# Optimization experiments

Hardware: AMD Instinct MI355X
Metric: run time of the kernel (lower is better)

Reference implementation:

```python
import jax, jax.numpy as jnp
import numpy as np

B, G, K, N, M, E, L = 8, 512, 64, 1024, 128, 4, 5

def _lin(x, w, b):
    return x @ w.T + b

def setup_inputs():
    key = jax.random.key(0)
    ks = jax.random.split(key, 20)
    def nrm(k, shape, s=1.0):
        return jax.random.normal(k, shape, dtype=jnp.float32) * s
    def lin_p(k, out_d, in_d):
        k1, k2 = jax.random.split(k)
        s = 1.0 / float(np.sqrt(in_d))
        return nrm(k1, (out_d, in_d), s), nrm(k2, (out_d,), s)
    inp = {}
    inp["z"] = nrm(ks[0], (B, G, K, M), 0.5)
    inp["hs_grid"] = nrm(ks[1], (B, G, M))
    inp["hs_key"] = nrm(ks[2], (B, K, M))
    inp["lig_rep"] = nrm(ks[3], (B, E))
    inp["hs_rec"] = nrm(ks[4], (B, N, M))
    inp["w_Rl"] = jnp.ones((1,), dtype=jnp.float32)
    inp["w_mask"] = jax.random.randint(ks[5], (B, K), 0, 2)
    dims = {"wra": (M, M), "wrh": (M, M), "wla": (M, M), "wlh": (M, M),
            "z1": (1, M), "wcR": (M, M), "wcl": (M, M), "kR": (M, M),
            "mapL": (L, 2 * M + E), "fin": (1, L)}
    for i, nm in enumerate(dims):
        w, b = lin_p(ks[6 + i], *dims[nm])
        inp[nm + "_w"] = w
        inp[nm + "_b"] = b
    return inp

def reference(z, hs_grid, hs_key, lig_rep, hs_rec, w_Rl, w_mask,
              wra_w, wra_b, wrh_w, wrh_b, wla_w, wla_b, wlh_w, wlh_b,
              z1_w, z1_b, wcR_w, wcR_b, wcl_w, wcl_b, kR_w, kR_b,
              mapL_w, mapL_b, fin_w, fin_b):
    exp_z = jnp.exp(z)                                    # [B,G,K,M]
    zr = exp_z / exp_z.sum(axis=-2, keepdims=True)        # pseudo-softmax over K
    ra = jnp.einsum('bgkm,bkm->bgm', zr, hs_key)          # [B,G,M]
    zl = exp_z / exp_z.sum(axis=-3, keepdims=True)        # pseudo-softmax over G
    la = jnp.einsum('bgkm,bgm->bkm', zl, hs_grid)         # [B,K,M]
    ra_rh = _lin(ra, wra_w, wra_b) + _lin(hs_grid, wrh_w, wrh_b)  # [B,G,M]
    la_lh = _lin(la, wla_w, wla_b) + _lin(hs_key, wlh_w, wlh_b)   # [B,K,M]
    att = _lin(z, z1_w, z1_b)[..., 0]                     # [B,G,K]
    att_l = jax.nn.softmax(att, axis=2).sum(axis=1)       # [B,K]
    att_r = jax.nn.softmax(att, axis=1).sum(axis=2)       # [B,G]
    key_rep = jnp.einsum('bk,bkm->bm', att_l, la_lh)      # [B,M]
    grid_rep = jnp.einsum('bg,bgm->bm', att_r, ra_rh)     # [B,M]
    Rh = _lin(hs_rec, wcR_w, wcR_b)                       # [B,N,M]
    lh = _lin(hs_key, wcl_w, wcl_b)                       # [B,K,M]
    z_Rl = jnp.einsum('bnh,bkh->bnk', Rh, lh)             # [B,N,K]
    masked = jnp.where(w_mask[:, None, :] == 0, jnp.float32(-1e10), w_Rl * z_Rl)
    z_Rl = jax.nn.softmax(masked, axis=1)                 # softmax over N
    kfr = jnp.einsum('bnk,bnh->bkh', z_Rl, hs_rec)        # [B,K,M]
    kfr = _lin(kfr, kR_w, kR_b)
    kfr = jnp.einsum('bk,bkh->bh', att_l, kfr)            # [B,M]
    key_rep = key_rep + kfr
    pair_rep = jnp.concatenate([key_rep, lig_rep, grid_rep], axis=1)  # [B,2M+E]
    pair_rep = _lin(pair_rep, mapL_w, mapL_b)             # [B,L]
    return _lin(pair_rep, fin_w, fin_b)[..., 0]           # [B]
```

## Files before the change

kernel.cpp:

```cpp
#include <hip/hip_runtime.h>

#define Bb 8
#define Gg 512
#define Kk 64
#define Nn 1024
#define Mm 128
#define KM (Kk * Mm)
#define GPB 16
#define NCH (Gg / GPB)

struct P7 { const float* p[7]; };

__global__ __launch_bounds__(1024) void kA(
    const float* __restrict__ z, const float* __restrict__ hs_grid,
    const float* __restrict__ hs_key, const float* __restrict__ z1w,
    P7 ptrs, float* __restrict__ wT,
    float* __restrict__ raOut, float* __restrict__ attOut,
    float* __restrict__ laNum, float* __restrict__ laDen)
{
  __shared__ __align__(16) float smem[18432];
  const int bid = blockIdx.x;
  const int t = threadIdx.x;

  if (bid >= Bb * NCH) {
    float* tile = smem;
    const int r = bid - Bb * NCH;
    const int mat = r >> 4, tl = r & 15;
    const int xo = (tl & 3) * 32, y0 = (tl >> 2) * 32;
    const int tx = t & 31, ty = t >> 5;
    const float* src = ptrs.p[mat];
    float* dst = wT + (size_t)mat * Mm * Mm;
    tile[ty * 33 + tx] = src[(size_t)(y0 + ty) * Mm + xo + tx];
    __syncthreads();
    dst[(size_t)(xo + ty) * Mm + y0 + tx] = tile[tx * 33 + ty];
    return;
  }

  float* s_hskey  = smem;
  float* s_hsgrid = smem + 8192;
  float* s_rn     = smem + 10240;
  float* s_rd     = smem + 14336;

  const int b = bid >> 5;
  const int gblk = bid & 31;
  const int lane_m = t & 31;
  const int m4 = lane_m << 2;
  const int kgrp = t >> 5;
  const int wv = t >> 6;

  const float* hkb = hs_key + (size_t)b * KM;
  for (int idx = t; idx < KM; idx += 1024) s_hskey[idx] = hkb[idx];
  const float* hgb = hs_grid + ((size_t)b * Gg + gblk * GPB) * Mm;
  for (int idx = t; idx < GPB * Mm; idx += 1024) s_hsgrid[idx] = hgb[idx];

  const float zw0 = z1w[m4], zw1 = z1w[m4 + 1], zw2 = z1w[m4 + 2], zw3 = z1w[m4 + 3];

  float la_n[2][4], la_d[2][4];
#pragma unroll
  for (int i = 0; i < 2; ++i)
#pragma unroll
    for (int j = 0; j < 4; ++j) { la_n[i][j] = 0.f; la_d[i][j] = 0.f; }

  const float* zb = z + ((size_t)b * Gg + gblk * GPB) * (size_t)Mm * Kk;
  const int ofs0 = (kgrp * 2) * Mm + m4;
  const int ofs1 = ofs0 + Mm;
  float4 c0 = *reinterpret_cast<const float4*>(zb + ofs0);
  float4 c1 = *reinterpret_cast<const float4*>(zb + ofs1);

  __syncthreads();

  for (int gl = 0; gl < GPB; ++gl) {
    float4 n0 = c0, n1 = c1;
    if (gl < GPB - 1) {
      n0 = *reinterpret_cast<const float4*>(zb + (size_t)(gl + 1) * KM + ofs0);
      n1 = *reinterpret_cast<const float4*>(zb + (size_t)(gl + 1) * KM + ofs1);
    }
    const int g = gblk * GPB + gl;
    const float4 hg = *reinterpret_cast<const float4*>(s_hsgrid + gl * Mm + m4);
    float rn0 = 0, rn1 = 0, rn2 = 0, rn3 = 0, rd0 = 0, rd1 = 0, rd2 = 0, rd3 = 0;
#pragma unroll
    for (int i = 0; i < 2; ++i) {
      const float4 v = (i == 0) ? c0 : c1;
      const int k = kgrp * 2 + i;
      const float e0 = __expf(v.x), e1 = __expf(v.y), e2 = __expf(v.z), e3 = __expf(v.w);
      la_n[i][0] += e0 * hg.x; la_n[i][1] += e1 * hg.y; la_n[i][2] += e2 * hg.z; la_n[i][3] += e3 * hg.w;
      la_d[i][0] += e0;        la_d[i][1] += e1;        la_d[i][2] += e2;        la_d[i][3] += e3;
      const float4 hk = *reinterpret_cast<const float4*>(s_hskey + k * Mm + m4);
      rn0 += e0 * hk.x; rn1 += e1 * hk.y; rn2 += e2 * hk.z; rn3 += e3 * hk.w;
      rd0 += e0; rd1 += e1; rd2 += e2; rd3 += e3;
      float ap = v.x * zw0 + v.y * zw1 + v.z * zw2 + v.w * zw3;
      ap += __shfl_xor(ap, 16); ap += __shfl_xor(ap, 8); ap += __shfl_xor(ap, 4);
      ap += __shfl_xor(ap, 2);  ap += __shfl_xor(ap, 1);
      if (lane_m == 0) attOut[((size_t)b * Gg + g) * Kk + k] = ap;
    }
    rn0 += __shfl_xor(rn0, 32); rn1 += __shfl_xor(rn1, 32); rn2 += __shfl_xor(rn2, 32); rn3 += __shfl_xor(rn3, 32);
    rd0 += __shfl_xor(rd0, 32); rd1 += __shfl_xor(rd1, 32); rd2 += __shfl_xor(rd2, 32); rd3 += __shfl_xor(rd3, 32);
    float* rnB = s_rn + (gl & 1) * 2048;
    float* rdB = s_rd + (gl & 1) * 2048;
    if ((t & 63) < 32) {
      *reinterpret_cast<float4*>(rnB + wv * Mm + m4) = make_float4(rn0, rn1, rn2, rn3);
      *reinterpret_cast<float4*>(rdB + wv * Mm + m4) = make_float4(rd0, rd1, rd2, rd3);
    }
    __syncthreads();
    if (t < Mm) {
      float num = 0.f, den = 0.f;
#pragma unroll
      for (int ww = 0; ww < 16; ++ww) { num += rnB[ww * Mm + t]; den += rdB[ww * Mm + t]; }
      raOut[((size_t)b * Gg + g) * Mm + t] = num / den;
    }
    c0 = n0; c1 = n1;
  }

  const size_t base = ((size_t)(b * NCH + gblk)) * KM;
#pragma unroll
  for (int i = 0; i < 2; ++i) {
    const int k = kgrp * 2 + i;
    *reinterpret_cast<float4*>(laNum + base + k * Mm + m4) =
        make_float4(la_n[i][0], la_n[i][1], la_n[i][2], la_n[i][3]);
    *reinterpret_cast<float4*>(laDen + base + k * Mm + m4) =
        make_float4(la_d[i][0], la_d[i][1], la_d[i][2], la_d[i][3]);
  }
}

__device__ __forceinline__ void lin1_body(
    int r0, const float* __restrict__ in1, const float* __restrict__ W1T,
    const float* __restrict__ b1, float* __restrict__ out, float* smem)
{
  float* s1 = smem;
  float* sacc = smem + 2048;
  const int t = threadIdx.x;
  const int m = t & 127, hh = t >> 7;
  for (int idx = t; idx < 2048; idx += 256) s1[idx] = in1[(size_t)r0 * Mm + idx];
  __syncthreads();
  float acc[16];
#pragma unroll
  for (int r = 0; r < 16; ++r) acc[r] = 0.f;
  const int h0 = hh * 64;
  for (int h = h0; h < h0 + 64; ++h) {
    const float w1 = W1T[(size_t)h * Mm + m];
#pragma unroll
    for (int r = 0; r < 16; ++r) acc[r] += s1[r * Mm + h] * w1;
  }
  if (hh == 1) {
#pragma unroll
    for (int r = 0; r < 16; ++r) sacc[r * Mm + m] = acc[r];
  }
  __syncthreads();
  if (hh == 0) {
    const float bias = b1[m];
#pragma unroll
    for (int r = 0; r < 16; ++r) out[(size_t)(r0 + r) * Mm + m] = acc[r] + sacc[r * Mm + m] + bias;
  }
}

__global__ __launch_bounds__(256) void kB(
    const float* __restrict__ laNum, const float* __restrict__ laDen, float* __restrict__ la,
    const float* __restrict__ att, float* __restrict__ attlP,
    float* __restrict__ attrPM, float* __restrict__ attrPS,
    const float* __restrict__ hs_rec, const float* __restrict__ hs_key,
    const float* __restrict__ wT, const float* __restrict__ wcR_b, const float* __restrict__ wcl_b,
    float* __restrict__ Rh, float* __restrict__ lh)
{
  __shared__ __align__(16) float smem[4096];
  const int bid = blockIdx.x;
  const int t = threadIdx.x;

  if (bid < 256) {
    const int idx = bid * 256 + t;
    const int b = idx >> 13, r = idx & 8191;
    const float* np = laNum + (size_t)b * NCH * KM + r;
    const float* dp = laDen + (size_t)b * NCH * KM + r;
    float num = 0.f, den = 0.f;
#pragma unroll 8
    for (int p = 0; p < NCH; ++p) { num += np[(size_t)p * KM]; den += dp[(size_t)p * KM]; }
    la[idx] = num / den;
  } else if (bid < 320) {
    const int blk = bid - 256;
    const int b = blk >> 3, p = blk & 7;
    const int w = t >> 6, lane = t & 63;
    float acc = 0.f;
    for (int j = 0; j < 16; ++j) {
      const int g = p * 64 + w * 16 + j;
      const float a = att[((size_t)b * Gg + g) * Kk + lane];
      float mx = a;
      for (int off = 32; off; off >>= 1) mx = fmaxf(mx, __shfl_xor(mx, off));
      const float e = __expf(a - mx);
      float s = e;
      for (int off = 32; off; off >>= 1) s += __shfl_xor(s, off);
      acc += e / s;
    }
    float* sred = smem;
    sred[w * 64 + lane] = acc;
    __syncthreads();
    if (t < 64) attlP[(b * 8 + p) * 64 + t] = sred[t] + sred[64 + t] + sred[128 + t] + sred[192 + t];
  } else if (bid < 384) {
    const int blk = bid - 320;
    const int b = blk >> 3, gc = blk & 7;
    const int k = t & 63, j4 = t >> 6;
    float m = -1e30f, s = 0.f;
    for (int j = 0; j < 16; ++j) {
      const int g = gc * 64 + j4 * 16 + j;
      const float a = att[((size_t)b * Gg + g) * Kk + k];
      if (a > m) { s = s * __expf(m - a) + 1.0f; m = a; }
      else s += __expf(a - m);
    }
    float* sm = smem;
    float* ss = smem + 256;
    sm[j4 * 64 + k] = m; ss[j4 * 64 + k] = s;
    __syncthreads();
    if (t < 64) {
      float M = sm[t];
      for (int q = 1; q < 4; ++q) M = fmaxf(M, sm[q * 64 + t]);
      float S = 0.f;
      for (int q = 0; q < 4; ++q) S += ss[q * 64 + t] * __expf(sm[q * 64 + t] - M);
      attrPM[(b * 8 + gc) * 64 + t] = M;
      attrPS[(b * 8 + gc) * 64 + t] = S;
    }
  } else if (bid < 896) {
    lin1_body((bid - 384) * 16, hs_rec, wT + 4 * 16384, wcR_b, Rh, smem);
  } else {
    lin1_body((bid - 896) * 16, hs_key, wT + 5 * 16384, wcl_b, lh, smem);
  }
}

__global__ __launch_bounds__(256) void kC(
    const float* __restrict__ att, const float* __restrict__ attrPM, const float* __restrict__ attrPS,
    float* __restrict__ att_r,
    const float* __restrict__ Rh, const float* __restrict__ lh,
    const int* __restrict__ mask, const float* __restrict__ wRl,
    float* __restrict__ scores, float* __restrict__ pmT, float* __restrict__ psT)
{
  __shared__ __align__(16) float smem[14912];
  const int bid = blockIdx.x;
  const int t = threadIdx.x;

  if (bid < 64) {
    const int b = bid >> 3, gc = bid & 7;
    const int k = t & 63, grp = t >> 6;
    float* Mx = smem;
    float* S = smem + 64;
    if (t < 64) {
      float M = -1e30f;
      for (int p = 0; p < 8; ++p) M = fmaxf(M, attrPM[(b * 8 + p) * 64 + t]);
      float s = 0.f;
      for (int p = 0; p < 8; ++p) s += attrPS[(b * 8 + p) * 64 + t] * __expf(attrPM[(b * 8 + p) * 64 + t] - M);
      Mx[t] = M; S[t] = s;
    }
    __syncthreads();
    const float Mk = Mx[k], Sk = S[k];
    for (int j = 0; j < 16; ++j) {
      const int g = gc * 64 + grp * 16 + j;
      float p = __expf(att[((size_t)b * Gg + g) * Kk + k] - Mk) / Sk;
      for (int off = 32; off; off >>= 1) p += __shfl_xor(p, off);
      if (k == 0) att_r[b * Gg + g] = p;
    }
  } else {
    const int vb = bid - 64;
    const int b = vb >> 6, ntile = vb & 63;
    const int n0 = ntile * 16;
    const int k = t & 63, hs = t >> 6;
    float* s_rh  = smem;
    float* s_lh  = smem + 2048;
    float* s_acc = smem + 10304;
    float* s_m   = smem + 14400;
    float* s_s   = smem + 14656;
    for (int idx = t; idx < 2048; idx += 256)
      s_rh[idx] = Rh[((size_t)b * Nn + n0) * Mm + idx];
    for (int idx = t; idx < 8192; idx += 256)
      s_lh[(idx >> 7) * 129 + (idx & 127)] = lh[(size_t)b * Kk * Mm + idx];
    __syncthreads();
    float acc[16];
#pragma unroll
    for (int r = 0; r < 16; ++r) acc[r] = 0.f;
    for (int h = hs * 32; h < hs * 32 + 32; ++h) {
      const float lv = s_lh[k * 129 + h];
#pragma unroll
      for (int r = 0; r < 16; ++r) acc[r] += s_rh[r * Mm + h] * lv;
    }
#pragma unroll
    for (int r = 0; r < 16; ++r) s_acc[(hs * 16 + r) * 64 + k] = acc[r];
    __syncthreads();
    const float wv = wRl[0];
    const bool msk = (mask[b * Kk + k] == 0);
    float m = -3.0e38f, ssum = 0.f;
    for (int q = 0; q < 4; ++q) {
      const int idx = q * 256 + t;
      const int r = idx >> 6, kk = idx & 63;
      float v = s_acc[r * 64 + kk] + s_acc[(16 + r) * 64 + kk] +
                s_acc[(32 + r) * 64 + kk] + s_acc[(48 + r) * 64 + kk];
      v = msk ? -1e10f : wv * v;
      scores[((size_t)b * Nn + n0 + r) * Kk + kk] = v;
      if (v > m) { ssum = ssum * __expf(m - v) + 1.0f; m = v; }
      else ssum += __expf(v - m);
    }
    s_m[hs * 64 + k] = m; s_s[hs * 64 + k] = ssum;
    __syncthreads();
    if (t < 64) {
      float M = fmaxf(fmaxf(s_m[t], s_m[64 + t]), fmaxf(s_m[128 + t], s_m[192 + t]));
      float S = 0.f;
#pragma unroll
      for (int q = 0; q < 4; ++q) S += s_s[q * 64 + t] * __expf(s_m[q * 64 + t] - M);
      pmT[((size_t)b * 64 + ntile) * 64 + t] = M;
      psT[((size_t)b * 64 + ntile) * 64 + t] = S;
    }
  }
}

__global__ __launch_bounds__(512) void kD(
    const float* __restrict__ scores, const float* __restrict__ hs_rec,
    const float* __restrict__ pmT, const float* __restrict__ psT,
    const float* __restrict__ attlP, const float* __restrict__ att_r,
    const float* __restrict__ ra, const float* __restrict__ hs_grid,
    const float* __restrict__ la, const float* __restrict__ hs_key,
    float* __restrict__ uP, float* __restrict__ w1P, float* __restrict__ w2P,
    float* __restrict__ w0P, float* __restrict__ v1, float* __restrict__ v2,
    float* __restrict__ sAv)
{
  __shared__ float sm[1280];
  __shared__ float s_attl[64];
  __shared__ float sM[64], sSi[64];
  const int bid = blockIdx.x;
  const int t = threadIdx.x;

  if (bid < 64) {
    const int b = bid >> 3, nc = bid & 7;
    if (t < 64) {
      float a = 0.f;
      for (int p = 0; p < 8; ++p) a += attlP[(b * 8 + p) * 64 + t];
      s_attl[t] = a;
      float M = -3.0e38f;
      for (int nt = 0; nt < 64; ++nt) M = fmaxf(M, pmT[((size_t)b * 64 + nt) * 64 + t]);
      float S = 0.f;
      for (int nt = 0; nt < 64; ++nt)
        S += psT[((size_t)b * 64 + nt) * 64 + t] * __expf(pmT[((size_t)b * 64 + nt) * 64 + t] - M);
      sM[t] = M; sSi[t] = 1.0f / S;
    }
    __syncthreads();
    const int n = t >> 2, ks = t & 3;
    const float* sc = scores + ((size_t)b * Nn + nc * 128 + n) * Kk + ks * 16;
    float qp = 0.f;
#pragma unroll
    for (int j = 0; j < 16; ++j) {
      const int k = ks * 16 + j;
      qp += s_attl[k] * __expf(sc[j] - sM[k]) * sSi[k];
    }
    sm[n * 4 + ks] = qp;
    __syncthreads();
    float* q = sm + 512;
    if (t < 128) q[t] = sm[t * 4] + sm[t * 4 + 1] + sm[t * 4 + 2] + sm[t * 4 + 3];
    __syncthreads();
    const int h = t & 127, nq = t >> 7;
    float acc = 0.f;
    const float* hr = hs_rec + ((size_t)b * Nn + nc * 128 + nq * 32) * Mm + h;
    for (int j = 0; j < 32; ++j) acc += q[nq * 32 + j] * hr[(size_t)j * Mm];
    float* red = sm + 640;
    red[nq * 128 + h] = acc;
    __syncthreads();
    if (t < 128) uP[((size_t)b * 8 + nc) * 128 + t] = red[t] + red[128 + t] + red[256 + t] + red[384 + t];
  } else if (bid < 128) {
    const int blk = bid - 64;
    const int b = blk >> 3, gc = blk & 7;
    float* s_ar = sm + 1152;
    if (t < 64) s_ar[t] = att_r[b * Gg + gc * 64 + t];
    __syncthreads();
    const int h = t & 127, gq = t >> 7;
    float a1 = 0.f, a2 = 0.f;
    const float* rp = ra + ((size_t)b * Gg + gc * 64 + gq * 16) * Mm + h;
    const float* gp = hs_grid + ((size_t)b * Gg + gc * 64 + gq * 16) * Mm + h;
    for (int j = 0; j < 16; ++j) {
      const float w = s_ar[gq * 16 + j];
      a1 += w * rp[(size_t)j * Mm];
      a2 += w * gp[(size_t)j * Mm];
    }
    float* r1 = sm;
    float* r2 = sm + 512;
    r1[gq * 128 + h] = a1; r2[gq * 128 + h] = a2;
    __syncthreads();
    if (t < 128) {
      w1P[((size_t)b * 8 + gc) * 128 + t] = r1[t] + r1[128 + t] + r1[256 + t] + r1[384 + t];
      w2P[((size_t)b * 8 + gc) * 128 + t] = r2[t] + r2[128 + t] + r2[256 + t] + r2[384 + t];
    }
    if (t == 0) {
      float s = 0.f;
      for (int j = 0; j < 64; ++j) s += s_ar[j];
      w0P[b * 8 + gc] = s;
    }
  } else {
    const int b = bid - 128;
    if (t < 64) {
      float a = 0.f;
      for (int p = 0; p < 8; ++p) a += attlP[(b * 8 + p) * 64 + t];
      s_attl[t] = a;
    }
    __syncthreads();
    const int h = t & 127, kq = t >> 7;
    float a1 = 0.f, a2 = 0.f;
    const float* lp = la + ((size_t)b * Kk + kq * 16) * Mm + h;
    const float* kp = hs_key + ((size_t)b * Kk + kq * 16) * Mm + h;
    for (int j = 0; j < 16; ++j) {
      const float w = s_attl[kq * 16 + j];
      a1 += w * lp[(size_t)j * Mm];
      a2 += w * kp[(size_t)j * Mm];
    }
    float* r1 = sm;
    float* r2 = sm + 512;
    r1[kq * 128 + h] = a1; r2[kq * 128 + h] = a2;
    __syncthreads();
    if (t < 128) {
      v1[b * 128 + t] = r1[t] + r1[128 + t] + r1[256 + t] + r1[384 + t];
      v2[b * 128 + t] = r2[t] + r2[128 + t] + r2[256 + t] + r2[384 + t];
    }
    if (t == 0) {
      float s = 0.f;
      for (int j = 0; j < 64; ++j) s += s_attl[j];
      sAv[b] = s;
    }
  }
}

__global__ __launch_bounds__(256) void kE(
    const float* __restrict__ uP, const float* __restrict__ w1P, const float* __restrict__ w2P,
    const float* __restrict__ w0P, const float* __restrict__ v1, const float* __restrict__ v2,
    const float* __restrict__ sAv, const float* __restrict__ wT,
    const float* __restrict__ wra_b, const float* __restrict__ wrh_b,
    const float* __restrict__ wla_b, const float* __restrict__ wlh_b,
    const float* __restrict__ kR_b, const float* __restrict__ lig_rep,
    const float* __restrict__ mapL_w, const float* __restrict__ mapL_b,
    const float* __restrict__ fin_w, const float* __restrict__ fin_b,
    float* __restrict__ out)
{
  __shared__ float sV1[128], sV2[128], sU[128], sW1[128], sW2[128];
  __shared__ float sPair[260];
  __shared__ float sRed[2][2][128];
  __shared__ float s5[8];
  __shared__ float sSc[2];
  const int b = blockIdx.x, t = threadIdx.x;
  const int m = t & 127, hf = t >> 7;

  if (t < 128) {
    float u = 0.f, w1 = 0.f, w2 = 0.f;
    for (int c = 0; c < 8; ++c) {
      u  += uP[((size_t)b * 8 + c) * 128 + t];
      w1 += w1P[((size_t)b * 8 + c) * 128 + t];
      w2 += w2P[((size_t)b * 8 + c) * 128 + t];
    }
    sU[t] = u; sW1[t] = w1; sW2[t] = w2;
    sV1[t] = v1[b * 128 + t]; sV2[t] = v2[b * 128 + t];
  }
  if (t == 0) {
    float s = 0.f;
    for (int c = 0; c < 8; ++c) s += w0P[b * 8 + c];
    sSc[0] = s;
    sSc[1] = sAv[b];
  }
  __syncthreads();

  const float* wraT = wT;
  const float* wrhT = wT + 1 * 16384;
  const float* wlaT = wT + 2 * 16384;
  const float* wlhT = wT + 3 * 16384;
  const float* kRT  = wT + 6 * 16384;
  float key = 0.f, grd = 0.f;
  for (int h = hf * 64; h < hf * 64 + 64; ++h) {
    key += sV1[h] * wlaT[h * Mm + m] + sV2[h] * wlhT[h * Mm + m] + sU[h] * kRT[h * Mm + m];
    grd += sW1[h] * wraT[h * Mm + m] + sW2[h] * wrhT[h * Mm + m];
  }
  sRed[0][hf][m] = key; sRed[1][hf][m] = grd;
  __syncthreads();
  if (t < 128) {
    const float sR = sSc[0], sA = sSc[1];
    sPair[t] = sRed[0][0][t] + sRed[0][1][t] + sA * (wla_b[t] + wlh_b[t] + kR_b[t]);
    sPair[132 + t] = sRed[1][0][t] + sRed[1][1][t] + sR * (wra_b[t] + wrh_b[t]);
  }
  if (t < 4) sPair[128 + t] = lig_rep[b * 4 + t];
  __syncthreads();

  const int wv = t >> 6, lane = t & 63;
  for (int l = wv; l < 5; l += 4) {
    float acc = 0.f;
    for (int c = lane; c < 260; c += 64) acc += sPair[c] * mapL_w[l * 260 + c];
    for (int off = 32; off; off >>= 1) acc += __shfl_xor(acc, off);
    if (lane == 0) s5[l] = acc + mapL_b[l];
  }
  __syncthreads();
  if (t == 0) {
    float o = fin_b[0];
    for (int l = 0; l < 5; ++l) o += s5[l] * fin_w[l];
    out[b] = o;
  }
}

extern "C" void kernel_launch(void* const* d_in, const int* in_sizes, int n_in,
                              void* d_out, int out_size, void* d_ws, size_t ws_size,
                              hipStream_t stream) {
  const float* z       = (const float*)d_in[0];
  const float* hs_grid = (const float*)d_in[1];
  const float* hs_key  = (const float*)d_in[2];
  const float* lig_rep = (const float*)d_in[3];
  const float* hs_rec  = (const float*)d_in[4];
  const float* w_Rl    = (const float*)d_in[5];
  const int*   w_mask  = (const int*)d_in[6];
  const float* wra_w = (const float*)d_in[7];  const float* wra_b = (const float*)d_in[8];
  const float* wrh_w = (const float*)d_in[9];  const float* wrh_b = (const float*)d_in[10];
  const float* wla_w = (const float*)d_in[11]; const float* wla_b = (const float*)d_in[12];
  const float* wlh_w = (const float*)d_in[13]; const float* wlh_b = (const float*)d_in[14];
  const float* z1_w  = (const float*)d_in[15];
  const float* wcR_w = (const float*)d_in[17]; const float* wcR_b = (const float*)d_in[18];
  const float* wcl_w = (const float*)d_in[19]; const float* wcl_b = (const float*)d_in[20];
  const float* kR_w  = (const float*)d_in[21]; const float* kR_b  = (const float*)d_in[22];
  const float* mapL_w = (const float*)d_in[23]; const float* mapL_b = (const float*)d_in[24];
  const float* fin_w  = (const float*)d_in[25]; const float* fin_b  = (const float*)d_in[26];
  float* out = (float*)d_out;

  float* w = (float*)d_ws;
  float* wT    = w;
  float* ra    = wT + 7 * 16384;
  float* att   = ra + Bb * Gg * Mm;
  float* laNum = att + Bb * Gg * Kk;
  float* laDen = laNum + Bb * NCH * Kk * Mm;
  float* la    = laDen + Bb * NCH * Kk * Mm;
  float* attlP = la + Bb * Kk * Mm;
  float* attrPM = attlP + Bb * 8 * 64;
  float* attrPS = attrPM + Bb * 8 * 64;
  float* att_r = attrPS + Bb * 8 * 64;
  float* Rh    = att_r + Bb * Gg;
  float* lh    = Rh + Bb * Nn * Mm;
  float* scores = lh + Bb * Kk * Mm;

  float* pmT  = laNum;
  float* psT  = laNum + 32768;
  float* uP   = laNum + 65536;
  float* w1P  = laNum + 73728;
  float* w2P  = laNum + 81920;
  float* w0P  = laNum + 90112;
  float* v1   = laNum + 90176;
  float* v2   = laNum + 91200;
  float* sAv  = laNum + 92224;

  P7 ptrs;
  ptrs.p[0] = wra_w; ptrs.p[1] = wrh_w; ptrs.p[2] = wla_w; ptrs.p[3] = wlh_w;
  ptrs.p[4] = wcR_w; ptrs.p[5] = wcl_w; ptrs.p[6] = kR_w;

  kA<<<Bb * NCH + 112, 1024, 0, stream>>>(z, hs_grid, hs_key, z1_w, ptrs, wT,
                                          ra, att, laNum, laDen);
  kB<<<928, 256, 0, stream>>>(laNum, laDen, la, att, attlP, attrPM, attrPS,
                              hs_rec, hs_key, wT, wcR_b, wcl_b, Rh, lh);
  kC<<<576, 256, 0, stream>>>(att, attrPM, attrPS, att_r, Rh, lh,
                              w_mask, w_Rl, scores, pmT, psT);
  kD<<<136, 512, 0, stream>>>(scores, hs_rec, pmT, psT, attlP, att_r,
                              ra, hs_grid, la, hs_key,
                              uP, w1P, w2P, w0P, v1, v2, sAv);
  kE<<<Bb, 256, 0, stream>>>(uP, w1P, w2P, w0P, v1, v2, sAv, wT,
                             wra_b, wrh_b, wla_b, wlh_b, kR_b, lig_rep,
                             mapL_w, mapL_b, fin_w, fin_b, out);
}
```

Measured before the change: 89.20 us.

## Reassociate receptor-key scores to skip projecting hs_rec through wcR

The scores are rewritten as hs_rec · (lh·wcR_w), so a small per-key matrix Lk of shape [B,K,M] is computed instead of the full [B,N,M] projection Rh. The wcR bias term is dropped. It only adds a per-(b,k) constant that cancels in the softmax over N, as long as the stored scores and their max/sum stay consistent. kB loses 480 blocks of GEMM work. kC now reads hs_rec directly from global memory with per-thread register copies of Lk, instead of staging both operands in shared memory. The trade-offs are less data reuse from LDS in kC and scores that differ numerically by that constant offset.

```diff
diff --git a/kernel.cpp b/kernel.cpp
--- a/kernel.cpp
+++ b/kernel.cpp
@@ -122,46 +122,15 @@
   }
 }
 
-__device__ __forceinline__ void lin1_body(
-    int r0, const float* __restrict__ in1, const float* __restrict__ W1T,
-    const float* __restrict__ b1, float* __restrict__ out, float* smem)
-{
-  float* s1 = smem;
-  float* sacc = smem + 2048;
-  const int t = threadIdx.x;
-  const int m = t & 127, hh = t >> 7;
-  for (int idx = t; idx < 2048; idx += 256) s1[idx] = in1[(size_t)r0 * Mm + idx];
-  __syncthreads();
-  float acc[16];
-#pragma unroll
-  for (int r = 0; r < 16; ++r) acc[r] = 0.f;
-  const int h0 = hh * 64;
-  for (int h = h0; h < h0 + 64; ++h) {
-    const float w1 = W1T[(size_t)h * Mm + m];
-#pragma unroll
-    for (int r = 0; r < 16; ++r) acc[r] += s1[r * Mm + h] * w1;
-  }
-  if (hh == 1) {
-#pragma unroll
-    for (int r = 0; r < 16; ++r) sacc[r * Mm + m] = acc[r];
-  }
-  __syncthreads();
-  if (hh == 0) {
-    const float bias = b1[m];
-#pragma unroll
-    for (int r = 0; r < 16; ++r) out[(size_t)(r0 + r) * Mm + m] = acc[r] + sacc[r * Mm + m] + bias;
-  }
-}
-
 __global__ __launch_bounds__(256) void kB(
     const float* __restrict__ laNum, const float* __restrict__ laDen, float* __restrict__ la,
     const float* __restrict__ att, float* __restrict__ attlP,
     float* __restrict__ attrPM, float* __restrict__ attrPS,
-    const float* __restrict__ hs_rec, const float* __restrict__ hs_key,
-    const float* __restrict__ wT, const float* __restrict__ wcR_b, const float* __restrict__ wcl_b,
-    float* __restrict__ Rh, float* __restrict__ lh)
+    const float* __restrict__ hs_key, const float* __restrict__ wT,
+    const float* __restrict__ wcR_w, const float* __restrict__ wcl_b,
+    float* __restrict__ Lk)
 {
-  __shared__ __align__(16) float smem[4096];
+  __shared__ __align__(16) float smem[1088];
   const int bid = blockIdx.x;
   const int t = threadIdx.x;
 
@@ -216,21 +185,63 @@
       attrPM[(b * 8 + gc) * 64 + t] = M;
       attrPS[(b * 8 + gc) * 64 + t] = S;
     }
-  } else if (bid < 896) {
-    lin1_body((bid - 384) * 16, hs_rec, wT + 4 * 16384, wcR_b, Rh, smem);
   } else {
-    lin1_body((bid - 896) * 16, hs_key, wT + 5 * 16384, wcl_b, lh, smem);
+    const int blk = bid - 384;
+    const int b = blk >> 3, k8 = blk & 7;
+    float* s_lh = smem;
+    const int m = t & 127;
+    const int half = __builtin_amdgcn_readfirstlane(t >> 7);
+    const float* wclT = wT + 5 * 16384;
+    {
+      const float* keyb = hs_key + ((size_t)b * Kk + k8 * 8 + half * 4) * Mm;
+      float a0 = 0.f, a1 = 0.f, a2 = 0.f, a3 = 0.f;
+      for (int h = 0; h < 128; ++h) {
+        const float w = wclT[(size_t)h * Mm + m];
+        const float r0v = keyb[h];
+        const float r1v = keyb[128 + h];
+        const float r2v = keyb[256 + h];
+        const float r3v = keyb[384 + h];
+        a0 += r0v * w; a1 += r1v * w; a2 += r2v * w; a3 += r3v * w;
+      }
+      const float bm = wcl_b[m];
+      s_lh[(half * 4 + 0) * 132 + m] = a0 + bm;
+      s_lh[(half * 4 + 1) * 132 + m] = a1 + bm;
+      s_lh[(half * 4 + 2) * 132 + m] = a2 + bm;
+      s_lh[(half * 4 + 3) * 132 + m] = a3 + bm;
+    }
+    __syncthreads();
+    {
+      const int h = m;
+      const int r0 = half * 4;
+      float b0 = 0.f, b1 = 0.f, b2 = 0.f, b3 = 0.f;
+      for (int mq = 0; mq < 32; ++mq) {
+        const float4 L0 = *reinterpret_cast<const float4*>(&s_lh[(r0 + 0) * 132 + mq * 4]);
+        const float4 L1 = *reinterpret_cast<const float4*>(&s_lh[(r0 + 1) * 132 + mq * 4]);
+        const float4 L2 = *reinterpret_cast<const float4*>(&s_lh[(r0 + 2) * 132 + mq * 4]);
+        const float4 L3 = *reinterpret_cast<const float4*>(&s_lh[(r0 + 3) * 132 + mq * 4]);
+        const float w0 = wcR_w[(size_t)(mq * 4 + 0) * Mm + h];
+        const float w1 = wcR_w[(size_t)(mq * 4 + 1) * Mm + h];
+        const float w2 = wcR_w[(size_t)(mq * 4 + 2) * Mm + h];
+        const float w3 = wcR_w[(size_t)(mq * 4 + 3) * Mm + h];
+        b0 += L0.x * w0 + L0.y * w1 + L0.z * w2 + L0.w * w3;
+        b1 += L1.x * w0 + L1.y * w1 + L1.z * w2 + L1.w * w3;
+        b2 += L2.x * w0 + L2.y * w1 + L2.z * w2 + L2.w * w3;
+        b3 += L3.x * w0 + L3.y * w1 + L3.z * w2 + L3.w * w3;
+      }
+      const size_t ob = ((size_t)b * Kk + k8 * 8 + r0) * Mm + h;
+      Lk[ob] = b0; Lk[ob + Mm] = b1; Lk[ob + 2 * Mm] = b2; Lk[ob + 3 * Mm] = b3;
+    }
   }
 }
 
 __global__ __launch_bounds__(256) void kC(
     const float* __restrict__ att, const float* __restrict__ attrPM, const float* __restrict__ attrPS,
     float* __restrict__ att_r,
-    const float* __restrict__ Rh, const float* __restrict__ lh,
+    const float* __restrict__ hs_rec, const float* __restrict__ Lk,
     const int* __restrict__ mask, const float* __restrict__ wRl,
     float* __restrict__ scores, float* __restrict__ pmT, float* __restrict__ psT)
 {
-  __shared__ __align__(16) float smem[14912];
+  __shared__ __align__(16) float smem[4608];
   const int bid = blockIdx.x;
   const int t = threadIdx.x;
 
@@ -258,27 +269,33 @@
     const int vb = bid - 64;
     const int b = vb >> 6, ntile = vb & 63;
     const int n0 = ntile * 16;
-    const int k = t & 63, hs = t >> 6;
-    float* s_rh  = smem;
-    float* s_lh  = smem + 2048;
-    float* s_acc = smem + 10304;
-    float* s_m   = smem + 14400;
-    float* s_s   = smem + 14656;
-    for (int idx = t; idx < 2048; idx += 256)
-      s_rh[idx] = Rh[((size_t)b * Nn + n0) * Mm + idx];
-    for (int idx = t; idx < 8192; idx += 256)
-      s_lh[(idx >> 7) * 129 + (idx & 127)] = lh[(size_t)b * Kk * Mm + idx];
-    __syncthreads();
+    const int k = t & 63;
+    const int hq = __builtin_amdgcn_readfirstlane(t >> 6);
+    float rLk[32];
+    {
+      const float* Lp = Lk + ((size_t)b * Kk + k) * Mm + hq * 32;
+#pragma unroll
+      for (int j = 0; j < 8; ++j) {
+        const float4 v = *reinterpret_cast<const float4*>(Lp + j * 4);
+        rLk[j * 4 + 0] = v.x; rLk[j * 4 + 1] = v.y;
+        rLk[j * 4 + 2] = v.z; rLk[j * 4 + 3] = v.w;
+      }
+    }
     float acc[16];
-#pragma unroll
-    for (int r = 0; r < 16; ++r) acc[r] = 0.f;
-    for (int h = hs * 32; h < hs * 32 + 32; ++h) {
-      const float lv = s_lh[k * 129 + h];
-#pragma unroll
-      for (int r = 0; r < 16; ++r) acc[r] += s_rh[r * Mm + h] * lv;
-    }
-#pragma unroll
-    for (int r = 0; r < 16; ++r) s_acc[(hs * 16 + r) * 64 + k] = acc[r];
+    const float* rb = hs_rec + ((size_t)b * Nn + n0) * Mm + hq * 32;
+#pragma unroll
+    for (int r = 0; r < 16; ++r) {
+      const float* rp = rb + r * Mm;
+      float s = 0.f;
+#pragma unroll
+      for (int j = 0; j < 32; ++j) s += rp[j] * rLk[j];
+      acc[r] = s;
+    }
+    float* s_acc = smem;
+    float* s_m   = smem + 4096;
+    float* s_s   = smem + 4352;
+#pragma unroll
+    for (int r = 0; r < 16; ++r) s_acc[(hq * 16 + r) * 64 + k] = acc[r];
     __syncthreads();
     const float wv = wRl[0];
     const bool msk = (mask[b * Kk + k] == 0);
@@ -293,7 +310,7 @@
       if (v > m) { ssum = ssum * __expf(m - v) + 1.0f; m = v; }
       else ssum += __expf(v - m);
     }
-    s_m[hs * 64 + k] = m; s_s[hs * 64 + k] = ssum;
+    s_m[hq * 64 + k] = m; s_s[hq * 64 + k] = ssum;
     __syncthreads();
     if (t < 64) {
       float M = fmaxf(fmaxf(s_m[t], s_m[64 + t]), fmaxf(s_m[128 + t], s_m[192 + t]));
@@ -523,9 +540,8 @@
   float* attrPM = attlP + Bb * 8 * 64;
   float* attrPS = attrPM + Bb * 8 * 64;
   float* att_r = attrPS + Bb * 8 * 64;
-  float* Rh    = att_r + Bb * Gg;
-  float* lh    = Rh + Bb * Nn * Mm;
-  float* scores = lh + Bb * Kk * Mm;
+  float* Lk    = att_r + Bb * Gg;
+  float* scores = Lk + Bb * Kk * Mm;
 
   float* pmT  = laNum;
   float* psT  = laNum + 32768;
@@ -543,9 +559,9 @@
 
   kA<<<Bb * NCH + 112, 1024, 0, stream>>>(z, hs_grid, hs_key, z1_w, ptrs, wT,
                                           ra, att, laNum, laDen);
-  kB<<<928, 256, 0, stream>>>(laNum, laDen, la, att, attlP, attrPM, attrPS,
-                              hs_rec, hs_key, wT, wcR_b, wcl_b, Rh, lh);
-  kC<<<576, 256, 0, stream>>>(att, attrPM, attrPS, att_r, Rh, lh,
+  kB<<<448, 256, 0, stream>>>(laNum, laDen, la, att, attlP, attrPM, attrPS,
+                              hs_key, wT, wcR_w, wcl_b, Lk);
+  kC<<<576, 256, 0, stream>>>(att, attrPM, attrPS, att_r, hs_rec, Lk,
                               w_mask, w_Rl, scores, pmT, psT);
   kD<<<136, 512, 0, stream>>>(scores, hs_rec, pmT, psT, attlP, att_r,
                               ra, hs_grid, la, hs_key,
```

Result: slower. 91.59 us (+2.7%).
